# Kernel optimization log

Measured on AMD Instinct MI355X. Metric: run time of the kernel, lower is better.

## Reference

```python
import jax, jax.numpy as jnp
import numpy as np

B, T, V, D, H = 256, 64, 6207, 512, 512  # batch, seq_len, vocab, emb_dim, hidden_dim
YF = 2048   # image feature dim -> concat with h (512) = 2560 gate input
EPS = 1e-10


def setup_inputs() -> dict:
    key = jax.random.key(0)
    ks = jax.random.split(key, 20)
    # torch init_parameters(): all params ~ U(-0.05, 0.05)
    u = lambda k, s: jax.random.uniform(k, s, jnp.float32, -0.05, 0.05)
    return {
        "y": jax.random.normal(ks[0], (B, YF), jnp.float32),
        "x": jax.random.randint(ks[1], (B, T), 0, V),
        "emb_w": u(ks[2], (V, D)),
        # bottom LSTM cell (input 512 -> hidden 512), torch layout: W_ih (4H, D)
        "W_ih": u(ks[3], (4 * H, D)), "W_hh": u(ks[4], (4 * H, H)),
        "b_ih": u(ks[5], (4 * H,)), "b_hh": u(ks[6], (4 * H,)),
        # top LSTM cell (input 512 -> hidden 512)
        "W_ih_t": u(ks[7], (4 * H, H)), "W_hh_t": u(ks[8], (4 * H, H)),
        "b_ih_t": u(ks[9], (4 * H,)), "b_hh_t": u(ks[10], (4 * H,)),
        # gate linear: Linear(2560, 512)
        "Wg": u(ks[11], (H, H + YF)), "bg": u(ks[12], (H,)),
        # final linear: Linear(512, 256)
        "Wlin": u(ks[13], (256, H)), "blin": u(ks[14], (256,)),
        # per-step gumbel-sigmoid uniforms (sampled inside forward in torch;
        # precomputed here so the reference is deterministic)
        "u1": jax.random.uniform(ks[15], (T, B, H), jnp.float32),
        "u2": jax.random.uniform(ks[16], (T, B, H), jnp.float32),
    }


def _lstm_cell(xt, h, c, Wi, Wh, bi, bh):
    # torch nn.LSTM gate order: i, f, g, o
    z = xt @ Wi.T + bi + h @ Wh.T + bh          # (B, 4H)
    i, f, g, o = jnp.split(z, 4, axis=-1)
    c = jax.nn.sigmoid(f) * c + jax.nn.sigmoid(i) * jnp.tanh(g)
    h = jax.nn.sigmoid(o) * jnp.tanh(c)
    return h, c


def reference(y, x, emb_w, W_ih, W_hh, b_ih, b_hh,
              W_ih_t, W_hh_t, b_ih_t, b_hh_t, Wg, bg, Wlin, blin, u1, u2):
    xs = jnp.transpose(emb_w[x], (1, 0, 2))     # (T, B, D)

    def step(carry, ins):
        h, c, ht, ct = carry
        xt, u1t, u2t = ins
        h, c = _lstm_cell(xt, h, c, W_ih, W_hh, b_ih, b_hh)
        # gate logits: relu(Linear([h, y]))
        logits = jax.nn.relu(jnp.concatenate([h, y], axis=1) @ Wg.T + bg)
        # custom gumbel-sigmoid noise: -log(log(U2+eps)/log(U1+eps)+eps)
        noise = -jnp.log(jnp.log(u2t + EPS) / jnp.log(u1t + EPS) + EPS)
        y_soft = jax.nn.sigmoid(logits + noise)
        # hard threshold at 0.5 with straight-through estimator
        y_hard = (y_soft >= 0.5).astype(y_soft.dtype)
        gate = y_hard - jax.lax.stop_gradient(y_soft) + y_soft
        hf = h * gate
        ht, ct = _lstm_cell(hf, ht, ct, W_ih_t, W_hh_t, b_ih_t, b_hh_t)
        return (h, c, ht, ct), None

    z0 = jnp.zeros((B, H), jnp.float32)
    (_, _, ht, _), _ = jax.lax.scan(step, (z0, z0, z0, z0), (xs, u1, u2))
    # dropout is identity in eval mode; torch output is (1, B, 256), squeezed here
    return jax.nn.relu(ht @ Wlin.T + blin)      # (B, 256)
```

## Files before the change

### kernel.cpp

```cpp
#include <hip/hip_runtime.h>
#include <hip/hip_bf16.h>


typedef __attribute__((ext_vector_type(8))) short short8;
typedef __attribute__((ext_vector_type(4))) float floatx4;
typedef __attribute__((ext_vector_type(4))) unsigned int uintx4;

#define MFMA16(a, b, c) __builtin_amdgcn_mfma_f32_16x16x32_bf16(a, b, c, 0, 0, 0)
#define AGENT __HIP_MEMORY_SCOPE_AGENT
#define HWREG_XCC_ID ((31u << 11) | (0u << 6) | 20u)

__device__ inline float bf2f(ushort u) {
    union { unsigned int u32; float f; } v; v.u32 = ((unsigned int)u) << 16; return v.f;
}
__device__ inline ushort f2bf(float f) {
    union { float f; unsigned int u; } v; v.f = f;
    return (ushort)((v.u + 0x7fffu + ((v.u >> 16) & 1u)) >> 16);
}
__device__ inline short8 ld8(const ushort* p) { return *(const short8*)p; }
__device__ inline float sigf(float x) { return 1.0f / (1.0f + expf(-x)); }
__device__ inline void mm3(floatx4& acc, short8 ah, short8 al, short8 bh, short8 bl) {
    acc = MFMA16(ah, bh, acc);
    acc = MFMA16(ah, bl, acc);
    acc = MFMA16(al, bh, acc);
}

__global__ __launch_bounds__(256) void k_prep(const float* __restrict__ w0,
                                              const float* __restrict__ w1,
                                              const float* __restrict__ w2,
                                              const float* __restrict__ w3,
                                              const float* __restrict__ wg,
                                              const float* __restrict__ wl,
                                              const float* __restrict__ em,
                                              const float* __restrict__ yy,
                                              ushort* __restrict__ wreg,
                                              uint* __restrict__ zbase) {
    unsigned i = blockIdx.x * 256u + threadIdx.x;
    if (i >= 9866784u) return;
    if (i >= 9338368u) {
        zbase[i - 9338368u] = 0u;
        return;
    }
    const float* src; ushort* hi; unsigned n, loc;
    if (i < 4194304u) {
        unsigned seg = i >> 20; loc = i & 1048575u; n = 1048576u;
        hi = wreg + seg * 2097152u;
        src = (seg == 0) ? w0 : (seg == 1) ? w1 : (seg == 2) ? w2 : w3;
    } else if (i < 5505024u) { loc = i - 4194304u; src = wg; hi = wreg + 8388608u;  n = 1310720u; }
    else if (i < 5636096u)   { loc = i - 5505024u; src = wl; hi = wreg + 11010048u; n = 131072u; }
    else if (i < 8814080u)   { loc = i - 5636096u; src = em; hi = wreg + 11272192u; n = 3177984u; }
    else                     { loc = i - 8814080u; src = yy; hi = wreg + 17628160u; n = 524288u; }
    float v = src[loc];
    ushort h = f2bf(v);
    hi[loc] = h;
    hi[n + loc] = f2bf(v - bf2f(h));
}

__global__ __launch_bounds__(512) void k_gy(const ushort* __restrict__ y_hi,
                                            const ushort* __restrict__ y_lo,
                                            const ushort* __restrict__ Wg_hi,
                                            const ushort* __restrict__ Wg_lo,
                                            const float* __restrict__ bg,
                                            float* __restrict__ gy) {
    __shared__ float zsB[4 * 528];
    int tid = threadIdx.x, lane = tid & 63, w = tid >> 6;
    int quad = lane >> 4, lr = lane & 15, q8 = quad * 8;
    int r0 = (blockIdx.x >> 4) * 16, n0 = (blockIdx.x & 15) * 32;
    int nh = w & 1, kq = w >> 1;
    int arow = r0 + lr, brow = n0 + nh * 16 + lr;
    floatx4 acc = {};
#pragma unroll
    for (int k0 = 0; k0 < 512; k0 += 32) {
        short8 ah = ld8(y_hi + arow * 2048 + kq * 512 + k0 + q8);
        short8 al = ld8(y_lo + arow * 2048 + kq * 512 + k0 + q8);
        short8 bh = ld8(Wg_hi + brow * 2560 + 512 + kq * 512 + k0 + q8);
        short8 bl = ld8(Wg_lo + brow * 2560 + 512 + kq * 512 + k0 + q8);
        mm3(acc, ah, al, bh, bl);
    }
#pragma unroll
    for (int r4 = 0; r4 < 4; r4++)
        zsB[kq * 528 + (quad * 4 + r4) * 33 + nh * 16 + lr] = acc[r4];
    __syncthreads();
    int ml = tid >> 5, jj = tid & 31;
    float s = zsB[ml * 33 + jj] + zsB[528 + ml * 33 + jj] +
              zsB[1056 + ml * 33 + jj] + zsB[1584 + ml * 33 + jj];
    gy[(r0 + ml) * 512 + n0 + jj] = s + bg[n0 + jj];
}

struct KP {
    const float *b_ih, *b_hh, *b_iht, *b_hht, *u1, *u2, *gy;
    const int* x;
    uint *hseq, *bseq;
    uint* claim;
    uint *hP0, *hP1, *htP0, *htP1, *bitsP;
    ushort *ht_hi, *ht_lo;
    const ushort *Whh_hi, *Whh_lo, *Wih_hi, *Wih_lo;
    const ushort *Wiht_hi, *Wiht_lo, *Whht_hi, *Whht_lo;
    const ushort *Wg_hi, *Wg_lo, *em_hi, *em_lo;
};

__device__ inline void publish(uint* sq, uint v) {
    asm volatile("" ::: "memory");
    __builtin_amdgcn_s_waitcnt(0);
    __syncthreads();
    if (threadIdx.x == 0)
        __hip_atomic_store(sq, v, __ATOMIC_RELAXED, AGENT);
}
__device__ inline void poll16(const uint* sq, uint target) {
    if ((threadIdx.x >> 6) == 0) {
        int l = threadIdx.x & 63;
        for (;;) {
            uint v = (l < 16) ? __hip_atomic_load(&sq[l], __ATOMIC_RELAXED, AGENT) : target;
            if (__all((int)(v >= target))) break;
            __builtin_amdgcn_s_sleep(1);
        }
    }
    __syncthreads();
}

__device__ inline void issue_row16(const uint* __restrict__ src, int r0, uintx4* v) {
    int tid = threadIdx.x;
    int sr = tid >> 5, scol = (tid & 31) * 16;
    const uint* pp = src + (r0 + sr) * 512 + scol;
    asm volatile(
        "global_load_dwordx4 %0, %4, off sc0 sc1\n\t"
        "global_load_dwordx4 %1, %4, off offset:16 sc0 sc1\n\t"
        "global_load_dwordx4 %2, %4, off offset:32 sc0 sc1\n\t"
        "global_load_dwordx4 %3, %4, off offset:48 sc0 sc1"
        : "=v"(v[0]), "=v"(v[1]), "=v"(v[2]), "=v"(v[3])
        : "v"(pp) : "memory");
}
__device__ inline void unpack_row16(const uintx4* v, ushort* __restrict__ dst) {
    int tid = threadIdx.x;
    int sr = tid >> 5, scol = (tid & 31) * 16;
    ushort* d = dst + sr * 1032;
#pragma unroll
    for (int i = 0; i < 4; i++) {
#pragma unroll
        for (int jp = 0; jp < 2; jp++) {
            uint u0 = v[i][jp * 2], u1v = v[i][jp * 2 + 1];
            int c = scol + i * 4 + jp * 2;
            *(uint*)(d + c) = (u0 & 0xffffu) | ((u1v & 0xffffu) << 16);
            *(uint*)(d + 520 + c) = (u0 >> 16) | (u1v & 0xffff0000u);
        }
    }
}

__device__ inline void stage_emb(const ushort* __restrict__ emh,
                                 const ushort* __restrict__ eml,
                                 const int* __restrict__ x, int r0, int t,
                                 ushort* __restrict__ dst) {
    int tid = threadIdx.x;
    int sr = tid >> 5, sc = (tid & 31) * 16;
    int tok = x[(r0 + sr) * 64 + t];
    const short8* ph = (const short8*)(emh + (size_t)tok * 512 + sc);
    const short8* pl = (const short8*)(eml + (size_t)tok * 512 + sc);
    short8 h0 = ph[0], h1 = ph[1], l0 = pl[0], l1 = pl[1];
    ushort* d = dst + sr * 1032;
    *(short8*)(d + sc) = h0;       *(short8*)(d + sc + 8) = h1;
    *(short8*)(d + 520 + sc) = l0; *(short8*)(d + 520 + sc + 8) = l1;
}

__device__ inline short8 fragA(const ushort* As, int row, int k) {
    return *(const short8*)(As + row * 1032 + k);
}

__global__ void __launch_bounds__(512, 1) k_main(KP p) {
    __shared__ ushort As[16 * 1032];
    __shared__ ushort Ae[16 * 1032];
    __shared__ ushort Az[16 * 1032];
    __shared__ ushort Ac[16 * 1032];
    __shared__ float zs[16 * 132];
    __shared__ uint gbits[256];
    __shared__ uint role_s;

    const int tid = threadIdx.x;
    const int w = tid >> 6;
    const int lane = tid & 63;
    const int quad = lane >> 4;
    const int lr = lane & 15;
    const int q8 = quad * 8;
    const float EPS = 1e-10f;

    if (tid == 0) {
        uint xcc = __builtin_amdgcn_s_getreg(HWREG_XCC_ID) & 7u;
        uint slot = __hip_atomic_fetch_add(&p.claim[xcc * 16], 1u,
                                           __ATOMIC_RELAXED, AGENT) & 31u;
        role_s = xcc * 32u + slot;
    }
    __syncthreads();
    const uint role = role_s;
    const int jb = (int)(role >> 4);
    const int g16 = (int)(role & 15u);
    const int r0 = g16 * 16, j0 = jb * 32;

    const int gate = w >> 1, nh = w & 1;
    const int brow = gate * 512 + j0 + nh * 16 + lr;
    const int kq = w >> 1;
    const int browB = j0 + nh * 16 + lr;
    const int ml = tid >> 5, jj = tid & 31;

    const float biasA = p.b_ih[brow] + p.b_hh[brow];
    const float biasC = p.b_iht[brow] + p.b_hht[brow];
    const float gy_r = p.gy[(r0 + ml) * 512 + j0 + jj];
    const ushort* WhhH = p.Whh_hi + brow * 512;
    const ushort* WhhL = p.Whh_lo + brow * 512;
    const ushort* WihH = p.Wih_hi + brow * 512;
    const ushort* WihL = p.Wih_lo + brow * 512;
    const ushort* WitH = p.Wiht_hi + brow * 512;
    const ushort* WitL = p.Wiht_lo + brow * 512;
    const ushort* WhtH = p.Whht_hi + brow * 512;
    const ushort* WhtL = p.Whht_lo + brow * 512;
    const ushort* WgH = p.Wg_hi + browB * 2560 + kq * 128;
    const ushort* WgL = p.Wg_lo + browB * 2560 + kq * 128;
    const float* pu1 = p.u1 + (r0 + ml) * 512 + j0 + jj;
    const float* pu2 = p.u2 + (r0 + ml) * 512 + j0 + jj;
    uint* hs = p.hseq + g16 * 16;
    uint* bs = p.bseq + g16 * 16;

    for (int i = tid; i < 16 * 1032; i += 512) As[i] = 0;
    stage_emb(p.em_hi, p.em_lo, p.x, r0, 0, Ae);
    __syncthreads();

    float c_reg = 0.0f, ct_reg = 0.0f;

    for (int t = 0; t < 64; t++) {
        {
            floatx4 a1 = {}, a2 = {};
#pragma unroll
            for (int k0 = 0; k0 < 512; k0 += 32) {
                mm3(a1, fragA(As, lr, k0 + q8), fragA(As, lr, 520 + k0 + q8),
                    ld8(WhhH + k0 + q8), ld8(WhhL + k0 + q8));
                mm3(a2, fragA(Ae, lr, k0 + q8), fragA(Ae, lr, 520 + k0 + q8),
                    ld8(WihH + k0 + q8), ld8(WihL + k0 + q8));
            }
#pragma unroll
            for (int r4 = 0; r4 < 4; r4++)
                zs[(quad * 4 + r4) * 132 + gate * 32 + nh * 16 + lr] =
                    a1[r4] + a2[r4] + biasA;
        }
        __syncthreads();
        uint* hPcur = (t & 1) ? p.hP1 : p.hP0;
        {
            float zi = zs[ml * 132 + jj],      zf = zs[ml * 132 + 32 + jj];
            float zg = zs[ml * 132 + 64 + jj], zo = zs[ml * 132 + 96 + jj];
            c_reg = sigf(zf) * c_reg + sigf(zi) * tanhf(zg);
            float hv = sigf(zo) * tanhf(c_reg);
            ushort hb = f2bf(hv);
            ushort lb = f2bf(hv - bf2f(hb));
            __hip_atomic_store(&hPcur[(r0 + ml) * 512 + j0 + jj],
                               (uint)hb | ((uint)lb << 16), __ATOMIC_RELAXED, AGENT);
        }
        publish(&hs[jb], (uint)(t + 1));
        float U1 = __builtin_nontemporal_load(pu1 + t * 131072);
        float U2 = __builtin_nontemporal_load(pu2 + t * 131072);
        float noise = -logf(logf(U2 + EPS) / logf(U1 + EPS) + EPS);
        poll16(hs, (uint)(t + 1));
        uintx4 va[4], vz[4];
        issue_row16(hPcur, r0, va);
        issue_row16((t & 1) ? p.htP0 : p.htP1, r0, vz);
        if (t < 63) stage_emb(p.em_hi, p.em_lo, p.x, r0, t + 1, Ae);
        asm volatile("s_waitcnt vmcnt(0)" ::: "memory");
        __builtin_amdgcn_sched_barrier(0);
        unpack_row16(va, As);
        unpack_row16(vz, Az);
        __syncthreads();

        {
            floatx4 acc = {};
#pragma unroll
            for (int k0 = 0; k0 < 128; k0 += 32)
                mm3(acc, fragA(As, lr, kq * 128 + k0 + q8),
                    fragA(As, lr, 520 + kq * 128 + k0 + q8),
                    ld8(WgH + k0 + q8), ld8(WgL + k0 + q8));
#pragma unroll
            for (int r4 = 0; r4 < 4; r4++)
                zs[kq * 528 + (quad * 4 + r4) * 33 + nh * 16 + lr] = acc[r4];
        }
        __syncthreads();
        {
            float z2 = zs[ml * 33 + jj] + zs[528 + ml * 33 + jj] +
                       zs[1056 + ml * 33 + jj] + zs[1584 + ml * 33 + jj];
            float logit = fmaxf(z2 + gy_r, 0.0f);
            bool gbit = sigf(logit + noise) >= 0.5f;
            unsigned long long bm = __ballot((int)gbit);
            if ((lane & 31) == 0)
                __hip_atomic_store(&p.bitsP[(r0 + ml) * 16 + jb],
                                   (uint)(bm >> ((lane >> 5) * 32)),
                                   __ATOMIC_RELAXED, AGENT);
        }
        publish(&bs[jb], (uint)(t + 1));

        floatx4 c2a = {};
#pragma unroll
        for (int k0 = 0; k0 < 256; k0 += 32)
            mm3(c2a, fragA(Az, lr, k0 + q8), fragA(Az, lr, 520 + k0 + q8),
                ld8(WhtH + k0 + q8), ld8(WhtL + k0 + q8));
        poll16(bs, (uint)(t + 1));
        uint rb = 0;
        if (tid < 256)
            asm volatile("global_load_dword %0, %1, off sc0 sc1"
                         : "=v"(rb) : "v"(p.bitsP + r0 * 16 + tid) : "memory");
#pragma unroll
        for (int k0 = 256; k0 < 512; k0 += 32)
            mm3(c2a, fragA(Az, lr, k0 + q8), fragA(Az, lr, 520 + k0 + q8),
                ld8(WhtH + k0 + q8), ld8(WhtL + k0 + q8));
        asm volatile("s_waitcnt vmcnt(0)" ::: "memory");
        __builtin_amdgcn_sched_barrier(0);
        if (tid < 256) gbits[tid] = rb;
        __syncthreads();
        {
            int sr = tid >> 5, sc = (tid & 31) * 16;
            uint word = gbits[sr * 16 + (sc >> 5)];
            uint chunk = (word >> (sc & 16)) & 0xffffu;
            const ushort* as0 = As + sr * 1032 + sc;
            ushort* ac0 = Ac + sr * 1032 + sc;
#pragma unroll
            for (int j = 0; j < 16; j++) {
                ushort m = (ushort)(0u - ((chunk >> j) & 1u));
                ac0[j] = (ushort)(as0[j] & m);
                ac0[520 + j] = (ushort)(as0[520 + j] & m);
            }
        }
        __syncthreads();
        {
            floatx4 c1a = {};
#pragma unroll
            for (int k0 = 0; k0 < 512; k0 += 32)
                mm3(c1a, fragA(Ac, lr, k0 + q8), fragA(Ac, lr, 520 + k0 + q8),
                    ld8(WitH + k0 + q8), ld8(WitL + k0 + q8));
#pragma unroll
            for (int r4 = 0; r4 < 4; r4++)
                zs[(quad * 4 + r4) * 132 + gate * 32 + nh * 16 + lr] =
                    c1a[r4] + c2a[r4] + biasC;
        }
        __syncthreads();
        {
            float zi = zs[ml * 132 + jj],      zf = zs[ml * 132 + 32 + jj];
            float zg = zs[ml * 132 + 64 + jj], zo = zs[ml * 132 + 96 + jj];
            ct_reg = sigf(zf) * ct_reg + sigf(zi) * tanhf(zg);
            float hv = sigf(zo) * tanhf(ct_reg);
            ushort hb = f2bf(hv);
            ushort lb = f2bf(hv - bf2f(hb));
            int idx = (r0 + ml) * 512 + j0 + jj;
            uint* htcur = (t & 1) ? p.htP1 : p.htP0;
            __hip_atomic_store(&htcur[idx], (uint)hb | ((uint)lb << 16),
                               __ATOMIC_RELAXED, AGENT);
            if (t == 63) { p.ht_hi[idx] = hb; p.ht_lo[idx] = lb; }
        }
        __syncthreads();
    }
}

__global__ __launch_bounds__(256) void k_final(const ushort* __restrict__ ht_hi,
                                               const ushort* __restrict__ ht_lo,
                                               const ushort* __restrict__ Wl_hi,
                                               const ushort* __restrict__ Wl_lo,
                                               const float* __restrict__ blin,
                                               float* __restrict__ out) {
    int tid = threadIdx.x, lane = tid & 63, w = tid >> 6;
    int wm = w & 1, wn = w >> 1, quad = lane >> 4, lr = lane & 15;
    int m0 = blockIdx.y * 64, n0 = blockIdx.x * 64;
    floatx4 acc[2][2] = {};
    for (int k0 = 0; k0 < 512; k0 += 32) {
        short8 ah[2], al[2], bh[2], bl[2];
#pragma unroll
        for (int tn = 0; tn < 2; tn++) {
            int n = n0 + wn * 32 + tn * 16 + lr;
            bh[tn] = ld8(Wl_hi + n * 512 + k0 + quad * 8);
            bl[tn] = ld8(Wl_lo + n * 512 + k0 + quad * 8);
        }
#pragma unroll
        for (int tm = 0; tm < 2; tm++) {
            int r = m0 + wm * 32 + tm * 16 + lr;
            ah[tm] = ld8(ht_hi + r * 512 + k0 + quad * 8);
            al[tm] = ld8(ht_lo + r * 512 + k0 + quad * 8);
        }
#pragma unroll
        for (int tm = 0; tm < 2; tm++)
#pragma unroll
            for (int tn = 0; tn < 2; tn++) mm3(acc[tm][tn], ah[tm], al[tm], bh[tn], bl[tn]);
    }
#pragma unroll
    for (int tm = 0; tm < 2; tm++)
#pragma unroll
        for (int tn = 0; tn < 2; tn++)
#pragma unroll
            for (int r4 = 0; r4 < 4; r4++) {
                int row = m0 + wm * 32 + tm * 16 + quad * 4 + r4;
                int n = n0 + wn * 32 + tn * 16 + lr;
                out[row * 256 + n] = fmaxf(acc[tm][tn][r4] + blin[n], 0.0f);
            }
}

extern "C" void kernel_launch(void* const* d_in, const int* in_sizes, int n_in,
                              void* d_out, int out_size, void* d_ws, size_t ws_size,
                              hipStream_t stream) {
    (void)in_sizes; (void)n_in; (void)out_size; (void)ws_size;
    const float* y      = (const float*)d_in[0];
    const int*   x      = (const int*)d_in[1];
    const float* emb    = (const float*)d_in[2];
    const float* W_ih   = (const float*)d_in[3];
    const float* W_hh   = (const float*)d_in[4];
    const float* b_ih   = (const float*)d_in[5];
    const float* b_hh   = (const float*)d_in[6];
    const float* W_iht  = (const float*)d_in[7];
    const float* W_hht  = (const float*)d_in[8];
    const float* b_iht  = (const float*)d_in[9];
    const float* b_hht  = (const float*)d_in[10];
    const float* Wg     = (const float*)d_in[11];
    const float* bg     = (const float*)d_in[12];
    const float* Wlin   = (const float*)d_in[13];
    const float* blin   = (const float*)d_in[14];
    const float* u1     = (const float*)d_in[15];
    const float* u2     = (const float*)d_in[16];
    float* out = (float*)d_out;

    uint* bar  = (uint*)d_ws;
    uint* hP0  = bar + 4128;
    uint* hP1  = hP0 + 131072;
    uint* htP0 = hP1 + 131072;
    uint* htP1 = htP0 + 131072;
    float* gy  = (float*)(htP1 + 131072);
    ushort* ht_hi = (ushort*)(gy + 131072);
    ushort* ht_lo = ht_hi + 131072;
    uint* bitsP = (uint*)(ht_lo + 131072);
    ushort* wreg = (ushort*)(bitsP + 4096);

    KP p;
    p.b_ih = b_ih; p.b_hh = b_hh; p.b_iht = b_iht; p.b_hht = b_hht;
    p.u1 = u1; p.u2 = u2; p.gy = gy; p.x = x;
    p.hseq = bar; p.bseq = bar + 256; p.claim = bar + 1024;
    p.hP0 = hP0; p.hP1 = hP1; p.htP0 = htP0; p.htP1 = htP1; p.bitsP = bitsP;
    p.ht_hi = ht_hi; p.ht_lo = ht_lo;
    p.Wih_hi  = wreg;             p.Wih_lo  = wreg + 1048576;
    p.Whh_hi  = wreg + 2097152;   p.Whh_lo  = wreg + 3145728;
    p.Wiht_hi = wreg + 4194304;   p.Wiht_lo = wreg + 5242880;
    p.Whht_hi = wreg + 6291456;   p.Whht_lo = wreg + 7340032;
    p.Wg_hi   = wreg + 8388608;   p.Wg_lo   = wreg + 9699328;
    p.em_hi   = wreg + 11272192;  p.em_lo   = wreg + 14450176;
    const ushort* Wl_hi = wreg + 11010048; const ushort* Wl_lo = wreg + 11141120;
    const ushort* y_hi  = wreg + 17628160; const ushort* y_lo  = wreg + 18152448;

    k_prep<<<dim3(38543), dim3(256), 0, stream>>>(W_ih, W_hh, W_iht, W_hht, Wg, Wlin,
                                                  emb, y, wreg, bar);
    k_gy<<<dim3(256), dim3(512), 0, stream>>>(y_hi, y_lo, p.Wg_hi, p.Wg_lo, bg, gy);

    void* args[] = {(void*)&p};
    hipLaunchCooperativeKernel((const void*)k_main, dim3(256), dim3(512), args, 0, stream);

    k_final<<<dim3(4, 4), dim3(256), 0, stream>>>(ht_hi, ht_lo, Wl_hi, Wl_lo, blin, out);
}
```

Measured before the change: 2.725 ms.

## Restructure LSTM step schedule with ht sequence flag and split top-cell recurrent GEMM

The bottom-cell GEMM is re-partitioned so one team of warps handles W_hh against h and the other handles W_ih against the embedding, with both partial sums reduced in shared memory. A new per-group tseq flag replaces the end-of-step barrier, so the ht exchange is waited on only when the next step needs it. The top-cell W_hh_t GEMM is split into three chunks placed inside the polling windows for h and the gate bits, and the embedding staging and the next step's noise loads are moved to later points. The goal is to hide cross-block synchronization latency behind MFMA work. The cost is a more complex dependency schedule and an extra flag array to maintain.

```diff
diff --git a/kernel.cpp b/kernel.cpp
--- a/kernel.cpp
+++ b/kernel.cpp
@@ -90,7 +90,7 @@
 struct KP {
     const float *b_ih, *b_hh, *b_iht, *b_hht, *u1, *u2, *gy;
     const int* x;
-    uint *hseq, *bseq;
+    uint *hseq, *bseq, *tseq;
     uint* claim;
     uint *hP0, *hP1, *htP0, *htP1, *bitsP;
     ushort *ht_hi, *ht_lo;
@@ -170,7 +170,7 @@
     __shared__ ushort Ae[16 * 1032];
     __shared__ ushort Az[16 * 1032];
     __shared__ ushort Ac[16 * 1032];
-    __shared__ float zs[16 * 132];
+    __shared__ float zsD[4224];
     __shared__ uint gbits[256];
     __shared__ uint role_s;
 
@@ -194,19 +194,26 @@
     const int g16 = (int)(role & 15u);
     const int r0 = g16 * 16, j0 = jb * 32;
 
+    const int g4 = w & 3, team = w >> 2;
     const int gate = w >> 1, nh = w & 1;
     const int brow = gate * 512 + j0 + nh * 16 + lr;
     const int kq = w >> 1;
     const int browB = j0 + nh * 16 + lr;
     const int ml = tid >> 5, jj = tid & 31;
 
-    const float biasA = p.b_ih[brow] + p.b_hh[brow];
-    const float biasC = p.b_iht[brow] + p.b_hht[brow];
+    const float biasAe0 = p.b_ih[j0 + jj]        + p.b_hh[j0 + jj];
+    const float biasAe1 = p.b_ih[512 + j0 + jj]  + p.b_hh[512 + j0 + jj];
+    const float biasAe2 = p.b_ih[1024 + j0 + jj] + p.b_hh[1024 + j0 + jj];
+    const float biasAe3 = p.b_ih[1536 + j0 + jj] + p.b_hh[1536 + j0 + jj];
+    const float biasCe0 = p.b_iht[j0 + jj]        + p.b_hht[j0 + jj];
+    const float biasCe1 = p.b_iht[512 + j0 + jj]  + p.b_hht[512 + j0 + jj];
+    const float biasCe2 = p.b_iht[1024 + j0 + jj] + p.b_hht[1024 + j0 + jj];
+    const float biasCe3 = p.b_iht[1536 + j0 + jj] + p.b_hht[1536 + j0 + jj];
     const float gy_r = p.gy[(r0 + ml) * 512 + j0 + jj];
-    const ushort* WhhH = p.Whh_hi + brow * 512;
-    const ushort* WhhL = p.Whh_lo + brow * 512;
-    const ushort* WihH = p.Wih_hi + brow * 512;
-    const ushort* WihL = p.Wih_lo + brow * 512;
+
+    const int rowA = g4 * 512 + j0 + lr;
+    const ushort* WAh = (team ? p.Wih_hi : p.Whh_hi) + rowA * 512;
+    const ushort* WAl = (team ? p.Wih_lo : p.Whh_lo) + rowA * 512;
     const ushort* WitH = p.Wiht_hi + brow * 512;
     const ushort* WitL = p.Wiht_lo + brow * 512;
     const ushort* WhtH = p.Whht_hi + brow * 512;
@@ -217,33 +224,42 @@
     const float* pu2 = p.u2 + (r0 + ml) * 512 + j0 + jj;
     uint* hs = p.hseq + g16 * 16;
     uint* bs = p.bseq + g16 * 16;
+    uint* hts = p.tseq + g16 * 16;
 
     for (int i = tid; i < 16 * 1032; i += 512) As[i] = 0;
     stage_emb(p.em_hi, p.em_lo, p.x, r0, 0, Ae);
+    float U1 = __builtin_nontemporal_load(pu1);
+    float U2 = __builtin_nontemporal_load(pu2);
     __syncthreads();
 
     float c_reg = 0.0f, ct_reg = 0.0f;
 
     for (int t = 0; t < 64; t++) {
         {
-            floatx4 a1 = {}, a2 = {};
+            const ushort* Ax = team ? Ae : As;
+            floatx4 acc0 = {}, acc1 = {};
 #pragma unroll
             for (int k0 = 0; k0 < 512; k0 += 32) {
-                mm3(a1, fragA(As, lr, k0 + q8), fragA(As, lr, 520 + k0 + q8),
-                    ld8(WhhH + k0 + q8), ld8(WhhL + k0 + q8));
-                mm3(a2, fragA(Ae, lr, k0 + q8), fragA(Ae, lr, 520 + k0 + q8),
-                    ld8(WihH + k0 + q8), ld8(WihL + k0 + q8));
+                short8 xh = fragA(Ax, lr, k0 + q8);
+                short8 xl = fragA(Ax, lr, 520 + k0 + q8);
+                mm3(acc0, xh, xl, ld8(WAh + k0 + q8), ld8(WAl + k0 + q8));
+                mm3(acc1, xh, xl, ld8(WAh + 8192 + k0 + q8), ld8(WAl + 8192 + k0 + q8));
             }
 #pragma unroll
-            for (int r4 = 0; r4 < 4; r4++)
-                zs[(quad * 4 + r4) * 132 + gate * 32 + nh * 16 + lr] =
-                    a1[r4] + a2[r4] + biasA;
-        }
-        __syncthreads();
+            for (int r4 = 0; r4 < 4; r4++) {
+                zsD[team * 2112 + (quad * 4 + r4) * 132 + g4 * 32 + lr]      = acc0[r4];
+                zsD[team * 2112 + (quad * 4 + r4) * 132 + g4 * 32 + 16 + lr] = acc1[r4];
+            }
+        }
+        if (t > 0) poll16(hts, (uint)t); else __syncthreads();
+        uintx4 vz[4];
+        issue_row16((t & 1) ? p.htP0 : p.htP1, r0, vz);
         uint* hPcur = (t & 1) ? p.hP1 : p.hP0;
         {
-            float zi = zs[ml * 132 + jj],      zf = zs[ml * 132 + 32 + jj];
-            float zg = zs[ml * 132 + 64 + jj], zo = zs[ml * 132 + 96 + jj];
+            float zi = (zsD[ml * 132 + jj]      + zsD[2112 + ml * 132 + jj])      + biasAe0;
+            float zf = (zsD[ml * 132 + 32 + jj] + zsD[2112 + ml * 132 + 32 + jj]) + biasAe1;
+            float zg = (zsD[ml * 132 + 64 + jj] + zsD[2112 + ml * 132 + 64 + jj]) + biasAe2;
+            float zo = (zsD[ml * 132 + 96 + jj] + zsD[2112 + ml * 132 + 96 + jj]) + biasAe3;
             c_reg = sigf(zf) * c_reg + sigf(zi) * tanhf(zg);
             float hv = sigf(zo) * tanhf(c_reg);
             ushort hb = f2bf(hv);
@@ -251,19 +267,28 @@
             __hip_atomic_store(&hPcur[(r0 + ml) * 512 + j0 + jj],
                                (uint)hb | ((uint)lb << 16), __ATOMIC_RELAXED, AGENT);
         }
-        publish(&hs[jb], (uint)(t + 1));
-        float U1 = __builtin_nontemporal_load(pu1 + t * 131072);
-        float U2 = __builtin_nontemporal_load(pu2 + t * 131072);
+        asm volatile("s_waitcnt vmcnt(0)" ::: "memory");
+        __builtin_amdgcn_sched_barrier(0);
+        unpack_row16(vz, Az);
+        __syncthreads();
+        if (tid == 0)
+            __hip_atomic_store(&hs[jb], (uint)(t + 1), __ATOMIC_RELAXED, AGENT);
         float noise = -logf(logf(U2 + EPS) / logf(U1 + EPS) + EPS);
+        floatx4 c2acc = {};
+#pragma unroll
+        for (int k0 = 0; k0 < 192; k0 += 32)
+            mm3(c2acc, fragA(Az, lr, k0 + q8), fragA(Az, lr, 520 + k0 + q8),
+                ld8(WhtH + k0 + q8), ld8(WhtL + k0 + q8));
         poll16(hs, (uint)(t + 1));
-        uintx4 va[4], vz[4];
+        uintx4 va[4];
         issue_row16(hPcur, r0, va);
-        issue_row16((t & 1) ? p.htP0 : p.htP1, r0, vz);
-        if (t < 63) stage_emb(p.em_hi, p.em_lo, p.x, r0, t + 1, Ae);
+#pragma unroll
+        for (int k0 = 192; k0 < 384; k0 += 32)
+            mm3(c2acc, fragA(Az, lr, k0 + q8), fragA(Az, lr, 520 + k0 + q8),
+                ld8(WhtH + k0 + q8), ld8(WhtL + k0 + q8));
         asm volatile("s_waitcnt vmcnt(0)" ::: "memory");
         __builtin_amdgcn_sched_barrier(0);
         unpack_row16(va, As);
-        unpack_row16(vz, Az);
         __syncthreads();
 
         {
@@ -275,12 +300,12 @@
                     ld8(WgH + k0 + q8), ld8(WgL + k0 + q8));
 #pragma unroll
             for (int r4 = 0; r4 < 4; r4++)
-                zs[kq * 528 + (quad * 4 + r4) * 33 + nh * 16 + lr] = acc[r4];
-        }
-        __syncthreads();
-        {
-            float z2 = zs[ml * 33 + jj] + zs[528 + ml * 33 + jj] +
-                       zs[1056 + ml * 33 + jj] + zs[1584 + ml * 33 + jj];
+                zsD[kq * 528 + (quad * 4 + r4) * 33 + nh * 16 + lr] = acc[r4];
+        }
+        __syncthreads();
+        {
+            float z2 = zsD[ml * 33 + jj] + zsD[528 + ml * 33 + jj] +
+                       zsD[1056 + ml * 33 + jj] + zsD[1584 + ml * 33 + jj];
             float logit = fmaxf(z2 + gy_r, 0.0f);
             bool gbit = sigf(logit + noise) >= 0.5f;
             unsigned long long bm = __ballot((int)gbit);
@@ -289,23 +314,27 @@
                                    (uint)(bm >> ((lane >> 5) * 32)),
                                    __ATOMIC_RELAXED, AGENT);
         }
+        if (t < 63) stage_emb(p.em_hi, p.em_lo, p.x, r0, t + 1, Ae);
         publish(&bs[jb], (uint)(t + 1));
-
-        floatx4 c2a = {};
-#pragma unroll
-        for (int k0 = 0; k0 < 256; k0 += 32)
-            mm3(c2a, fragA(Az, lr, k0 + q8), fragA(Az, lr, 520 + k0 + q8),
+#pragma unroll
+        for (int k0 = 384; k0 < 512; k0 += 32)
+            mm3(c2acc, fragA(Az, lr, k0 + q8), fragA(Az, lr, 520 + k0 + q8),
                 ld8(WhtH + k0 + q8), ld8(WhtL + k0 + q8));
+#pragma unroll
+        for (int r4 = 0; r4 < 4; r4++)
+            zsD[2112 + (quad * 4 + r4) * 132 + gate * 32 + nh * 16 + lr] = c2acc[r4];
         poll16(bs, (uint)(t + 1));
         uint rb = 0;
         if (tid < 256)
             asm volatile("global_load_dword %0, %1, off sc0 sc1"
                          : "=v"(rb) : "v"(p.bitsP + r0 * 16 + tid) : "memory");
-#pragma unroll
-        for (int k0 = 256; k0 < 512; k0 += 32)
-            mm3(c2a, fragA(Az, lr, k0 + q8), fragA(Az, lr, 520 + k0 + q8),
-                ld8(WhtH + k0 + q8), ld8(WhtL + k0 + q8));
-        asm volatile("s_waitcnt vmcnt(0)" ::: "memory");
+        if (t < 63) {
+            U1 = __builtin_nontemporal_load(pu1 + (t + 1) * 131072);
+            U2 = __builtin_nontemporal_load(pu2 + (t + 1) * 131072);
+            asm volatile("s_waitcnt vmcnt(2)" ::: "memory");
+        } else {
+            asm volatile("s_waitcnt vmcnt(0)" ::: "memory");
+        }
         __builtin_amdgcn_sched_barrier(0);
         if (tid < 256) gbits[tid] = rb;
         __syncthreads();
@@ -324,20 +353,21 @@
         }
         __syncthreads();
         {
-            floatx4 c1a = {};
+            floatx4 c1acc = {};
 #pragma unroll
             for (int k0 = 0; k0 < 512; k0 += 32)
-                mm3(c1a, fragA(Ac, lr, k0 + q8), fragA(Ac, lr, 520 + k0 + q8),
+                mm3(c1acc, fragA(Ac, lr, k0 + q8), fragA(Ac, lr, 520 + k0 + q8),
                     ld8(WitH + k0 + q8), ld8(WitL + k0 + q8));
 #pragma unroll
             for (int r4 = 0; r4 < 4; r4++)
-                zs[(quad * 4 + r4) * 132 + gate * 32 + nh * 16 + lr] =
-                    c1a[r4] + c2a[r4] + biasC;
-        }
-        __syncthreads();
-        {
-            float zi = zs[ml * 132 + jj],      zf = zs[ml * 132 + 32 + jj];
-            float zg = zs[ml * 132 + 64 + jj], zo = zs[ml * 132 + 96 + jj];
+                zsD[(quad * 4 + r4) * 132 + gate * 32 + nh * 16 + lr] = c1acc[r4];
+        }
+        __syncthreads();
+        {
+            float zi = (zsD[ml * 132 + jj]      + zsD[2112 + ml * 132 + jj])      + biasCe0;
+            float zf = (zsD[ml * 132 + 32 + jj] + zsD[2112 + ml * 132 + 32 + jj]) + biasCe1;
+            float zg = (zsD[ml * 132 + 64 + jj] + zsD[2112 + ml * 132 + 64 + jj]) + biasCe2;
+            float zo = (zsD[ml * 132 + 96 + jj] + zsD[2112 + ml * 132 + 96 + jj]) + biasCe3;
             ct_reg = sigf(zf) * ct_reg + sigf(zi) * tanhf(zg);
             float hv = sigf(zo) * tanhf(ct_reg);
             ushort hb = f2bf(hv);
@@ -348,7 +378,7 @@
                                __ATOMIC_RELAXED, AGENT);
             if (t == 63) { p.ht_hi[idx] = hb; p.ht_lo[idx] = lb; }
         }
-        __syncthreads();
+        publish(&hts[jb], (uint)(t + 1));
     }
 }
 
@@ -430,7 +460,7 @@
     KP p;
     p.b_ih = b_ih; p.b_hh = b_hh; p.b_iht = b_iht; p.b_hht = b_hht;
     p.u1 = u1; p.u2 = u2; p.gy = gy; p.x = x;
-    p.hseq = bar; p.bseq = bar + 256; p.claim = bar + 1024;
+    p.hseq = bar; p.bseq = bar + 256; p.tseq = bar + 512; p.claim = bar + 1024;
     p.hP0 = hP0; p.hP1 = hP1; p.htP0 = htP0; p.htP1 = htP1; p.bitsP = bitsP;
     p.ht_hi = ht_hi; p.ht_lo = ht_lo;
     p.Wih_hi  = wreg;             p.Wih_lo  = wreg + 1048576;
```

Result: faster. 2.590 ms (-5.0%).
